# Optimization experiments

Hardware: AMD Instinct MI355X
Metric: run time of the kernel (lower is better)

The kernel has to match this reference:

```python
import jax, jax.numpy as jnp
import numpy as np
from jax import lax

B, C, H, W = 8, 64, 128, 128
KS = 3          # kernel size
K = KS * KS     # kernel field = 9
PAD = 1


def conv2d(x, w, b):
    # x: [B,Cin,H,W], w: [Cout,Cin,kh,kw], 'same' 3x3 conv
    y = lax.conv_general_dilated(x, w, window_strides=(1, 1),
                                 padding=((PAD, PAD), (PAD, PAD)),
                                 dimension_numbers=('NCHW', 'OIHW', 'NCHW'))
    return y + b[None, :, None, None]


def modulated_deform_conv(x, offset, mask, weight, bias):
    # x:[B,C,H,W], offset:[B,2K,H,W] (dy,dx per tap), mask:[B,K,H,W]
    Bs, Cin, Hin, Win = x.shape
    off = offset.reshape(Bs, K, 2, Hin, Win)
    ky, kx = jnp.meshgrid(jnp.arange(KS), jnp.arange(KS), indexing='ij')
    ky = ky.reshape(K).astype(x.dtype)   # kernel tap row offsets 0..2
    kx = kx.reshape(K).astype(x.dtype)
    # sampling positions p = p0 + p_k + offset (stride=1, pad=1)
    py = (jnp.arange(Hin, dtype=x.dtype)[None, None, :, None] - PAD
          + ky[None, :, None, None] + off[:, :, 0])            # [B,K,H,W]
    px = (jnp.arange(Win, dtype=x.dtype)[None, None, None, :] - PAD
          + kx[None, :, None, None] + off[:, :, 1])            # [B,K,H,W]

    y0 = jnp.floor(py); x0 = jnp.floor(px)
    ly = py - y0; lx = px - x0                                  # frac parts
    y0i = y0.astype(jnp.int32); x0i = x0.astype(jnp.int32)

    x_flat = x.reshape(Bs, Cin, Hin * Win)

    def gather(iy, ix):
        valid = ((iy >= 0) & (iy < Hin) & (ix >= 0) & (ix < Win))
        flat = (jnp.clip(iy, 0, Hin - 1) * Win + jnp.clip(ix, 0, Win - 1))
        g = jax.vmap(lambda xb, ib: xb[:, ib])(x_flat, flat.reshape(Bs, -1))
        g = g.reshape(Bs, Cin, K, Hin, Win)
        return g * valid[:, None].astype(x.dtype)

    w00 = ((1 - ly) * (1 - lx))[:, None]  # [B,1,K,H,W]
    w01 = ((1 - ly) * lx)[:, None]
    w10 = (ly * (1 - lx))[:, None]
    w11 = (ly * lx)[:, None]

    val = (w00 * gather(y0i, x0i) + w01 * gather(y0i, x0i + 1)
           + w10 * gather(y0i + 1, x0i) + w11 * gather(y0i + 1, x0i + 1))
    val = val * mask[:, None]                                   # modulation
    out = jnp.einsum('ock,bckhw->bohw', weight.reshape(weight.shape[0], Cin, K), val)
    return out + bias[None, :, None, None]


def setup_inputs() -> dict:
    key = jax.random.key(0)
    ks = jax.random.split(key, 7)
    s = 0.05
    return {
        'x': jax.random.normal(ks[0], (B, C, H, W), jnp.float32),
        'w_om': jax.random.normal(ks[1], (3 * K, C, KS, KS), jnp.float32) * s,
        'b_om': jax.random.normal(ks[2], (3 * K,), jnp.float32) * s,
        'w_dc': jax.random.normal(ks[3], (C, C, KS, KS), jnp.float32) * s,
        'b_dc': jax.random.normal(ks[4], (C,), jnp.float32) * s,
        'w_c': jax.random.normal(ks[5], (C, C, KS, KS), jnp.float32) * s,
        'b_c': jax.random.normal(ks[6], (C,), jnp.float32) * s,
    }


def reference(x, w_om, b_om, w_dc, b_dc, w_c, b_c):
    om = conv2d(x, w_om, b_om)                       # [B,3K,H,W]
    offset, mask_raw = om[:, :2 * K], om[:, 2 * K:]
    mask = 2.0 * jax.nn.sigmoid(mask_raw)
    out = modulated_deform_conv(x, offset, mask, w_dc, b_dc)
    act = jnp.where(out > 0, out, 0.2 * out)         # LeakyReLU(0.2)
    return conv2d(act, w_c, b_c) + x
```

## Files before the change

kernel.cpp:

```cpp
#include <hip/hip_runtime.h>
#include <math.h>

#define Bn 8
#define Cn 64
#define Hn 128
#define Wn 128
#define HWn (Hn * Wn)
#define Kn 9

#define XSW 36
#define XSROW (66 * XSW)
#define XSCC (3 * XSROW)
#define VSTRIDE 292

#define WOM_OFF 0
#define WDC_OFF 18432
#define WC_OFF 55296

typedef __attribute__((ext_vector_type(8))) short short8;
typedef __attribute__((ext_vector_type(4))) float floatx4;

__device__ __forceinline__ float bf2f(short s) {
  return __uint_as_float(((unsigned)(unsigned short)s) << 16);
}
__device__ __forceinline__ short f2bf(float f) {
  unsigned u = __float_as_uint(f);
  u += 0x7fff + ((u >> 16) & 1);
  return (short)(u >> 16);
}

__global__ __launch_bounds__(256) void k_prep_w(
    const float* __restrict__ w_om, const float* __restrict__ w_dc,
    const float* __restrict__ w_c, short* __restrict__ wt) {
  int idx = blockIdx.x * 256 + threadIdx.x;
  if (idx >= 92160) return;
  float v;
  if (idx < WDC_OFF) {
    int e = idx;
    int elem = e & 7, lane = (e >> 3) & 63, mt = (e >> 9) & 1, t = e >> 10;
    int kk = t % 9, cc = t / 9;
    int row = mt * 16 + (lane & 15);
    int cin = cc * 32 + (lane >> 4) * 8 + elem;
    v = (row < 27) ? w_om[(row * 64 + cin) * 9 + kk] : 0.f;
  } else {
    int e = (idx < WC_OFF) ? idx - WDC_OFF : idx - WC_OFF;
    const float* src = (idx < WC_OFF) ? w_dc : w_c;
    int elem = e & 7, lane = (e >> 3) & 63, mt = (e >> 9) & 3, t = e >> 11;
    int kk = t % 9, cc = t / 9;
    int row = mt * 16 + (lane & 15);
    int cin = cc * 32 + (lane >> 4) * 8 + elem;
    v = src[(row * 64 + cin) * 9 + kk];
  }
  wt[idx] = f2bf(v);
}

__global__ __launch_bounds__(256) void k_prep_x(const float* __restrict__ x,
                                                short* __restrict__ xT) {
  __shared__ float tile[64][129];
  const int bid = blockIdx.x;
  const int b = bid & 7, h = bid >> 3;
  const int tid = threadIdx.x;
  const float* xb = x + (size_t)b * 64 * HWn + h * Wn;
  for (int i = tid; i < 8192; i += 256) {
    int c = i >> 7, w = i & 127;
    tile[c][w] = xb[c * HWn + w];
  }
  __syncthreads();
  short* dst = xT + ((size_t)(b * Hn + h) * Wn) * 64;
  for (int i = tid; i < 2048; i += 256) {
    int w = i >> 4, c4 = (i & 15) * 4;
    short4 o;
    o.x = f2bf(tile[c4 + 0][w]);
    o.y = f2bf(tile[c4 + 1][w]);
    o.z = f2bf(tile[c4 + 2][w]);
    o.w = f2bf(tile[c4 + 3][w]);
    *(short4*)(dst + (size_t)w * 64 + c4) = o;
  }
}

__global__ __launch_bounds__(256, 3) void k_omdef(
    const short* __restrict__ xT, const short* __restrict__ wt,
    const float* __restrict__ b_om, const float* __restrict__ b_dc,
    short* __restrict__ actT) {
  __shared__ __attribute__((aligned(16))) char raw[64 * VSTRIDE * 2 + 9216];
  short* xs = (short*)raw;
  float* som = (float*)(raw + XSCC * 2);
  short(*val)[VSTRIDE] = (short(*)[VSTRIDE])raw;
  unsigned* sbw = (unsigned*)(raw + 64 * VSTRIDE * 2);
  unsigned* sb01 = sbw, *sb23 = sbw + 576, *sw01 = sbw + 1152,
          *sw23 = sbw + 1728;

  const int bid = blockIdx.x;
  const int b = bid & 7;
  const int r = bid >> 3;
  const int h = r >> 1, w0 = (r & 1) * 64;
  const int tid = threadIdx.x;
  const int wave = tid >> 6, lane = tid & 63, quad = lane >> 4, lr = lane & 15;
  const short* xb = xT + (size_t)b * HWn * 64;

  floatx4 zf = {0.f, 0.f, 0.f, 0.f};
  floatx4 aco0 = zf, aco1 = zf;
  const int mto = wave & 1;
  const int n0 = (wave >> 1) * 32;

  for (int cc = 0; cc < 2; ++cc) {
    if (cc) __syncthreads();
    for (int j = tid; j < 792; j += 256) {
      int c8 = (j & 3) * 8;
      int rr = j >> 2;
      int ky = rr / 66, p = rr - ky * 66;
      int gy = h + ky - 1, gx = w0 - 1 + p;
      short8 v = {0, 0, 0, 0, 0, 0, 0, 0};
      if (gy >= 0 && gy < Hn && gx >= 0 && gx < Wn)
        v = *(const short8*)(xb + (size_t)(gy * Wn + gx) * 64 + cc * 32 + c8);
      *(short8*)(xs + ky * XSROW + p * XSW + c8) = v;
    }
    __syncthreads();
#pragma unroll
    for (int kk = 0; kk < 9; ++kk) {
      int ky = kk / 3, kx = kk - ky * 3;
      short8 a = *(const short8*)(wt + WOM_OFF +
                                  (((cc * 9 + kk) * 2 + mto) * 64 + lane) * 8);
      const short* bp = xs + ky * XSROW + kx * XSW + quad * 8;
      short8 b0 = *(const short8*)(bp + (n0 + lr) * XSW);
      short8 b1 = *(const short8*)(bp + (n0 + 16 + lr) * XSW);
      aco0 = __builtin_amdgcn_mfma_f32_16x16x32_bf16(a, b0, aco0, 0, 0, 0);
      aco1 = __builtin_amdgcn_mfma_f32_16x16x32_bf16(a, b1, aco1, 0, 0, 0);
    }
  }
#pragma unroll
  for (int nt = 0; nt < 2; ++nt) {
    floatx4 a = nt ? aco1 : aco0;
    int px = n0 + nt * 16 + lr;
#pragma unroll
    for (int rr = 0; rr < 4; ++rr) {
      int co = mto * 16 + quad * 4 + rr;
      if (co < 27) {
        float v = a[rr] + b_om[co];
        if (co >= 18) v = 2.f / (1.f + expf(-v));
        som[co * 65 + px] = v;
      }
    }
  }
  __syncthreads();

  for (int pr = tid; pr < 576; pr += 256) {
    int k = pr >> 6, p = pr & 63;
    float offy = som[(2 * k) * 65 + p];
    float offx = som[(2 * k + 1) * 65 + p];
    float m = som[(18 + k) * 65 + p];
    float py = (float)(h - 1 + (k / 3)) + offy;
    float px_ = (float)(w0 + p - 1 + (k % 3)) + offx;
    float fy = floorf(py), fx = floorf(px_);
    float ly = py - fy, lx = px_ - fx;
    int iy0 = (int)fy, ix0 = (int)fx;
    int iy1 = iy0 + 1, ix1 = ix0 + 1;
    bool vy0 = (iy0 >= 0) && (iy0 < Hn);
    bool vy1 = (iy1 >= 0) && (iy1 < Hn);
    bool vx0 = (ix0 >= 0) && (ix0 < Wn);
    bool vx1 = (ix1 >= 0) && (ix1 < Wn);
    unsigned cy0 = (unsigned)min(max(iy0, 0), Hn - 1);
    unsigned cy1 = (unsigned)min(max(iy1, 0), Hn - 1);
    unsigned cx0 = (unsigned)min(max(ix0, 0), Wn - 1);
    unsigned cx1 = (unsigned)min(max(ix1, 0), Wn - 1);
    sb01[pr] = (cy0 * Wn + cx0) | ((cy0 * Wn + cx1) << 16);
    sb23[pr] = (cy1 * Wn + cx0) | ((cy1 * Wn + cx1) << 16);
    float u0 = (vy0 && vx0) ? (1.f - ly) * (1.f - lx) * m : 0.f;
    float u1 = (vy0 && vx1) ? (1.f - ly) * lx * m : 0.f;
    float u2 = (vy1 && vx0) ? ly * (1.f - lx) * m : 0.f;
    float u3 = (vy1 && vx1) ? ly * lx * m : 0.f;
    sw01[pr] = (unsigned)(unsigned short)f2bf(u0) |
               ((unsigned)(unsigned short)f2bf(u1) << 16);
    sw23[pr] = (unsigned)(unsigned short)f2bf(u2) |
               ((unsigned)(unsigned short)f2bf(u3) << 16);
  }
  __syncthreads();

  floatx4 acc[2][2] = {{zf, zf}, {zf, zf}};
  const int mt0 = (wave & 1) * 2;

  for (int cc = 0; cc < 2; ++cc) {
    if (cc) __syncthreads();
    for (int j = tid; j < 2304; j += 256) {
      int chunk = j & 3, pr = j >> 2;
      int p = pr & 63, k = pr >> 6;
      unsigned a01 = sb01[pr], a23 = sb23[pr];
      unsigned uw01 = sw01[pr], uw23 = sw23[pr];
      float u0 = bf2f((short)(uw01 & 0xFFFF));
      float u1 = bf2f((short)(uw01 >> 16));
      float u2 = bf2f((short)(uw23 & 0xFFFF));
      float u3 = bf2f((short)(uw23 >> 16));
      int co = cc * 32 + chunk * 8;
      short8 q0 = *(const short8*)(xb + (size_t)(a01 & 0xFFFF) * 64 + co);
      short8 q1 = *(const short8*)(xb + (size_t)(a01 >> 16) * 64 + co);
      short8 q2 = *(const short8*)(xb + (size_t)(a23 & 0xFFFF) * 64 + co);
      short8 q3 = *(const short8*)(xb + (size_t)(a23 >> 16) * 64 + co);
      short8 o;
#pragma unroll
      for (int e = 0; e < 8; ++e) {
        float f = u0 * bf2f(q0[e]) + u1 * bf2f(q1[e]) + u2 * bf2f(q2[e]) +
                  u3 * bf2f(q3[e]);
        o[e] = f2bf(f);
      }
      *(short8*)&val[p][k * 32 + chunk * 8] = o;
    }
    __syncthreads();
#pragma unroll
    for (int kk = 0; kk < 9; ++kk) {
      short8 a0 = *(const short8*)(wt + WDC_OFF +
                                   (((cc * 9 + kk) * 4 + mt0) * 64 + lane) * 8);
      short8 a1 = *(const short8*)(wt + WDC_OFF +
                                   (((cc * 9 + kk) * 4 + mt0 + 1) * 64 + lane) * 8);
      short8 b0 = *(const short8*)&val[n0 + lr][kk * 32 + quad * 8];
      short8 b1 = *(const short8*)&val[n0 + 16 + lr][kk * 32 + quad * 8];
      acc[0][0] = __builtin_amdgcn_mfma_f32_16x16x32_bf16(a0, b0, acc[0][0], 0, 0, 0);
      acc[0][1] = __builtin_amdgcn_mfma_f32_16x16x32_bf16(a0, b1, acc[0][1], 0, 0, 0);
      acc[1][0] = __builtin_amdgcn_mfma_f32_16x16x32_bf16(a1, b0, acc[1][0], 0, 0, 0);
      acc[1][1] = __builtin_amdgcn_mfma_f32_16x16x32_bf16(a1, b1, acc[1][1], 0, 0, 0);
    }
  }

  short* ab = actT + ((size_t)(b * Hn + h) * Wn + w0) * 64;
#pragma unroll
  for (int mt = 0; mt < 2; ++mt) {
#pragma unroll
    for (int nt = 0; nt < 2; ++nt) {
      int px = n0 + nt * 16 + lr;
      int c0 = (mt0 + mt) * 16 + quad * 4;
      short4 o;
      float v;
      v = acc[mt][nt][0] + b_dc[c0 + 0]; o.x = f2bf(v > 0.f ? v : 0.2f * v);
      v = acc[mt][nt][1] + b_dc[c0 + 1]; o.y = f2bf(v > 0.f ? v : 0.2f * v);
      v = acc[mt][nt][2] + b_dc[c0 + 2]; o.z = f2bf(v > 0.f ? v : 0.2f * v);
      v = acc[mt][nt][3] + b_dc[c0 + 3]; o.w = f2bf(v > 0.f ? v : 0.2f * v);
      *(short4*)(ab + (size_t)px * 64 + c0) = o;
    }
  }
}

__global__ __launch_bounds__(256, 5) void k_conv_out(
    const short* __restrict__ actT, const short* __restrict__ wt,
    const float* __restrict__ b_c, const float* __restrict__ x,
    float* __restrict__ out) {
  __shared__ __attribute__((aligned(16))) short as_[2 * XSCC];

  const int bid = blockIdx.x;
  const int b = bid & 7;
  const int r = bid >> 3;
  const int h = r >> 1, w0 = (r & 1) * 64;
  const int tid = threadIdx.x;
  const int wave = tid >> 6, lane = tid & 63, quad = lane >> 4, lr = lane & 15;
  const short* ab = actT + (size_t)b * HWn * 64;

  for (int j = tid; j < 1584; j += 256) {
    int cc = j / 792, rr = j - cc * 792;
    int c8 = (rr & 3) * 8;
    int r2 = rr >> 2;
    int ky = r2 / 66, p = r2 - ky * 66;
    int gy = h + ky - 1, gx = w0 - 1 + p;
    short8 v = {0, 0, 0, 0, 0, 0, 0, 0};
    if (gy >= 0 && gy < Hn && gx >= 0 && gx < Wn)
      v = *(const short8*)(ab + (size_t)(gy * Wn + gx) * 64 + cc * 32 + c8);
    *(short8*)(as_ + cc * XSCC + ky * XSROW + p * XSW + c8) = v;
  }
  __syncthreads();

  floatx4 zf = {0.f, 0.f, 0.f, 0.f};
  floatx4 acc[2][2] = {{zf, zf}, {zf, zf}};
  const int mt0 = (wave & 1) * 2;
  const int n0 = (wave >> 1) * 32;

  for (int cc = 0; cc < 2; ++cc) {
#pragma unroll
    for (int kk = 0; kk < 9; ++kk) {
      int ky = kk / 3, kx = kk - ky * 3;
      short8 a0 = *(const short8*)(wt + WC_OFF +
                                   (((cc * 9 + kk) * 4 + mt0) * 64 + lane) * 8);
      short8 a1 = *(const short8*)(wt + WC_OFF +
                                   (((cc * 9 + kk) * 4 + mt0 + 1) * 64 + lane) * 8);
      const short* bp = as_ + cc * XSCC + ky * XSROW + kx * XSW + quad * 8;
      short8 b0 = *(const short8*)(bp + (n0 + lr) * XSW);
      short8 b1 = *(const short8*)(bp + (n0 + 16 + lr) * XSW);
      acc[0][0] = __builtin_amdgcn_mfma_f32_16x16x32_bf16(a0, b0, acc[0][0], 0, 0, 0);
      acc[0][1] = __builtin_amdgcn_mfma_f32_16x16x32_bf16(a0, b1, acc[0][1], 0, 0, 0);
      acc[1][0] = __builtin_amdgcn_mfma_f32_16x16x32_bf16(a1, b0, acc[1][0], 0, 0, 0);
      acc[1][1] = __builtin_amdgcn_mfma_f32_16x16x32_bf16(a1, b1, acc[1][1], 0, 0, 0);
    }
  }

#pragma unroll
  for (int mt = 0; mt < 2; ++mt) {
#pragma unroll
    for (int nt = 0; nt < 2; ++nt) {
      int px = n0 + nt * 16 + lr;
#pragma unroll
      for (int rr = 0; rr < 4; ++rr) {
        int cout = (mt0 + mt) * 16 + quad * 4 + rr;
        size_t gidx = ((size_t)(b * 64 + cout) * Hn + h) * Wn + w0 + px;
        out[gidx] = acc[mt][nt][rr] + b_c[cout] + x[gidx];
      }
    }
  }
}

extern "C" void kernel_launch(void* const* d_in, const int* in_sizes, int n_in,
                              void* d_out, int out_size, void* d_ws,
                              size_t ws_size, hipStream_t stream) {
  const float* x = (const float*)d_in[0];
  const float* w_om = (const float*)d_in[1];
  const float* b_om = (const float*)d_in[2];
  const float* w_dc = (const float*)d_in[3];
  const float* b_dc = (const float*)d_in[4];
  const float* w_c = (const float*)d_in[5];
  const float* b_c = (const float*)d_in[6];
  float* out = (float*)d_out;

  short* xT = (short*)d_ws;
  short* actT = xT + (size_t)Bn * HWn * 64;
  short* wt = actT + (size_t)Bn * HWn * 64;

  k_prep_w<<<dim3(360), 256, 0, stream>>>(w_om, w_dc, w_c, wt);
  k_prep_x<<<dim3(1024), 256, 0, stream>>>(x, xT);
  k_omdef<<<dim3(2048), 256, 0, stream>>>(xT, wt, b_om, b_dc, actT);
  k_conv_out<<<dim3(2048), 256, 0, stream>>>(actT, wt, b_c, x, out);
}
```

Measured before the change: 237.5 us.

## Drop LDS staging; feed MFMA B operands directly from global memory per wave

Both the offset/mask conv, the deformable sampling GEMM and the output conv now load their B operands straight from global (channel-last bf16) into registers instead of staging halo tiles and the sampled value matrix in shared memory. Each wave owns 16 pixels and all output-channel tiles, so the bilinear-interpolated samples go directly into MFMA inputs without an LDS round trip and the intra-loop barriers disappear. Shared memory shrinks to the offset/mask and sample-index tables, and occupancy hints are raised to 4 blocks. The tradeoff is that overlapping 3x3 neighborhoods are re-read through cache instead of being reused from LDS, and weight fragments are loaded redundantly by every wave.

```diff
diff --git a/kernel.cpp b/kernel.cpp
--- a/kernel.cpp
+++ b/kernel.cpp
@@ -6,12 +6,6 @@
 #define Hn 128
 #define Wn 128
 #define HWn (Hn * Wn)
-#define Kn 9
-
-#define XSW 36
-#define XSROW (66 * XSW)
-#define XSCC (3 * XSROW)
-#define VSTRIDE 292
 
 #define WOM_OFF 0
 #define WDC_OFF 18432
@@ -78,17 +72,16 @@
   }
 }
 
-__global__ __launch_bounds__(256, 3) void k_omdef(
+__global__ __launch_bounds__(256, 4) void k_omdef(
     const short* __restrict__ xT, const short* __restrict__ wt,
     const float* __restrict__ b_om, const float* __restrict__ b_dc,
     short* __restrict__ actT) {
-  __shared__ __attribute__((aligned(16))) char raw[64 * VSTRIDE * 2 + 9216];
-  short* xs = (short*)raw;
-  float* som = (float*)(raw + XSCC * 2);
-  short(*val)[VSTRIDE] = (short(*)[VSTRIDE])raw;
-  unsigned* sbw = (unsigned*)(raw + 64 * VSTRIDE * 2);
-  unsigned* sb01 = sbw, *sb23 = sbw + 576, *sw01 = sbw + 1152,
-          *sw23 = sbw + 1728;
+  __shared__ float som[27 * 66];
+  __shared__ unsigned sbw[4 * 576];
+  unsigned* sb01 = sbw;
+  unsigned* sb23 = sbw + 576;
+  unsigned* sw01 = sbw + 1152;
+  unsigned* sw23 = sbw + 1728;
 
   const int bid = blockIdx.x;
   const int b = bid & 7;
@@ -97,48 +90,38 @@
   const int tid = threadIdx.x;
   const int wave = tid >> 6, lane = tid & 63, quad = lane >> 4, lr = lane & 15;
   const short* xb = xT + (size_t)b * HWn * 64;
+  const int pxl = wave * 16 + lr;
+  const int gxp = w0 + pxl;
 
   floatx4 zf = {0.f, 0.f, 0.f, 0.f};
-  floatx4 aco0 = zf, aco1 = zf;
-  const int mto = wave & 1;
-  const int n0 = (wave >> 1) * 32;
-
-  for (int cc = 0; cc < 2; ++cc) {
-    if (cc) __syncthreads();
-    for (int j = tid; j < 792; j += 256) {
-      int c8 = (j & 3) * 8;
-      int rr = j >> 2;
-      int ky = rr / 66, p = rr - ky * 66;
-      int gy = h + ky - 1, gx = w0 - 1 + p;
-      short8 v = {0, 0, 0, 0, 0, 0, 0, 0};
-      if (gy >= 0 && gy < Hn && gx >= 0 && gx < Wn)
-        v = *(const short8*)(xb + (size_t)(gy * Wn + gx) * 64 + cc * 32 + c8);
-      *(short8*)(xs + ky * XSROW + p * XSW + c8) = v;
-    }
-    __syncthreads();
-#pragma unroll
-    for (int kk = 0; kk < 9; ++kk) {
-      int ky = kk / 3, kx = kk - ky * 3;
-      short8 a = *(const short8*)(wt + WOM_OFF +
-                                  (((cc * 9 + kk) * 2 + mto) * 64 + lane) * 8);
-      const short* bp = xs + ky * XSROW + kx * XSW + quad * 8;
-      short8 b0 = *(const short8*)(bp + (n0 + lr) * XSW);
-      short8 b1 = *(const short8*)(bp + (n0 + 16 + lr) * XSW);
-      aco0 = __builtin_amdgcn_mfma_f32_16x16x32_bf16(a, b0, aco0, 0, 0, 0);
-      aco1 = __builtin_amdgcn_mfma_f32_16x16x32_bf16(a, b1, aco1, 0, 0, 0);
-    }
-  }
-#pragma unroll
-  for (int nt = 0; nt < 2; ++nt) {
-    floatx4 a = nt ? aco1 : aco0;
-    int px = n0 + nt * 16 + lr;
+
+  floatx4 aco[2] = {zf, zf};
+  for (int kk = 0; kk < 9; ++kk) {
+    int ky = kk / 3, kx = kk - ky * 3;
+    int gy = h + ky - 1, gx = gxp + kx - 1;
+    bool ok = ((unsigned)gy < (unsigned)Hn) && ((unsigned)gx < (unsigned)Wn);
+    int gyc = min(max(gy, 0), Hn - 1), gxc = min(max(gx, 0), Wn - 1);
+    const short* rec = xb + (size_t)(gyc * Wn + gxc) * 64 + quad * 8;
+#pragma unroll
+    for (int cc = 0; cc < 2; ++cc) {
+      short8 bf = *(const short8*)(rec + cc * 32);
+      if (!ok) bf = (short8){0, 0, 0, 0, 0, 0, 0, 0};
+      const short* ap = wt + WOM_OFF + (size_t)((cc * 9 + kk) * 2) * 512 + lane * 8;
+      short8 a0 = *(const short8*)(ap);
+      short8 a1 = *(const short8*)(ap + 512);
+      aco[0] = __builtin_amdgcn_mfma_f32_16x16x32_bf16(a0, bf, aco[0], 0, 0, 0);
+      aco[1] = __builtin_amdgcn_mfma_f32_16x16x32_bf16(a1, bf, aco[1], 0, 0, 0);
+    }
+  }
+#pragma unroll
+  for (int mt = 0; mt < 2; ++mt) {
 #pragma unroll
     for (int rr = 0; rr < 4; ++rr) {
-      int co = mto * 16 + quad * 4 + rr;
+      int co = mt * 16 + quad * 4 + rr;
       if (co < 27) {
-        float v = a[rr] + b_om[co];
+        float v = aco[mt][rr] + b_om[co];
         if (co >= 18) v = 2.f / (1.f + expf(-v));
-        som[co * 65 + px] = v;
+        som[co * 66 + pxl] = v;
       }
     }
   }
@@ -146,9 +129,9 @@
 
   for (int pr = tid; pr < 576; pr += 256) {
     int k = pr >> 6, p = pr & 63;
-    float offy = som[(2 * k) * 65 + p];
-    float offx = som[(2 * k + 1) * 65 + p];
-    float m = som[(18 + k) * 65 + p];
+    float offy = som[(2 * k) * 66 + p];
+    float offx = som[(2 * k + 1) * 66 + p];
+    float m = som[(18 + k) * 66 + p];
     float py = (float)(h - 1 + (k / 3)) + offy;
     float px_ = (float)(w0 + p - 1 + (k % 3)) + offx;
     float fy = floorf(py), fx = floorf(px_);
@@ -176,74 +159,59 @@
   }
   __syncthreads();
 
-  floatx4 acc[2][2] = {{zf, zf}, {zf, zf}};
-  const int mt0 = (wave & 1) * 2;
-
-  for (int cc = 0; cc < 2; ++cc) {
-    if (cc) __syncthreads();
-    for (int j = tid; j < 2304; j += 256) {
-      int chunk = j & 3, pr = j >> 2;
-      int p = pr & 63, k = pr >> 6;
-      unsigned a01 = sb01[pr], a23 = sb23[pr];
-      unsigned uw01 = sw01[pr], uw23 = sw23[pr];
-      float u0 = bf2f((short)(uw01 & 0xFFFF));
-      float u1 = bf2f((short)(uw01 >> 16));
-      float u2 = bf2f((short)(uw23 & 0xFFFF));
-      float u3 = bf2f((short)(uw23 >> 16));
-      int co = cc * 32 + chunk * 8;
-      short8 q0 = *(const short8*)(xb + (size_t)(a01 & 0xFFFF) * 64 + co);
-      short8 q1 = *(const short8*)(xb + (size_t)(a01 >> 16) * 64 + co);
-      short8 q2 = *(const short8*)(xb + (size_t)(a23 & 0xFFFF) * 64 + co);
-      short8 q3 = *(const short8*)(xb + (size_t)(a23 >> 16) * 64 + co);
-      short8 o;
+  floatx4 acc[4] = {zf, zf, zf, zf};
+  for (int kk = 0; kk < 9; ++kk) {
+    int pr = kk * 64 + pxl;
+    unsigned a01 = sb01[pr], a23 = sb23[pr];
+    unsigned uw01 = sw01[pr], uw23 = sw23[pr];
+    float u0 = bf2f((short)(uw01 & 0xFFFF));
+    float u1 = bf2f((short)(uw01 >> 16));
+    float u2 = bf2f((short)(uw23 & 0xFFFF));
+    float u3 = bf2f((short)(uw23 >> 16));
+    const short* s0 = xb + (size_t)(a01 & 0xFFFF) * 64 + quad * 8;
+    const short* s1 = xb + (size_t)(a01 >> 16) * 64 + quad * 8;
+    const short* s2 = xb + (size_t)(a23 & 0xFFFF) * 64 + quad * 8;
+    const short* s3 = xb + (size_t)(a23 >> 16) * 64 + quad * 8;
+#pragma unroll
+    for (int cc = 0; cc < 2; ++cc) {
+      short8 q0 = *(const short8*)(s0 + cc * 32);
+      short8 q1 = *(const short8*)(s1 + cc * 32);
+      short8 q2 = *(const short8*)(s2 + cc * 32);
+      short8 q3 = *(const short8*)(s3 + cc * 32);
+      short8 bf;
 #pragma unroll
       for (int e = 0; e < 8; ++e) {
         float f = u0 * bf2f(q0[e]) + u1 * bf2f(q1[e]) + u2 * bf2f(q2[e]) +
                   u3 * bf2f(q3[e]);
-        o[e] = f2bf(f);
-      }
-      *(short8*)&val[p][k * 32 + chunk * 8] = o;
-    }
-    __syncthreads();
-#pragma unroll
-    for (int kk = 0; kk < 9; ++kk) {
-      short8 a0 = *(const short8*)(wt + WDC_OFF +
-                                   (((cc * 9 + kk) * 4 + mt0) * 64 + lane) * 8);
-      short8 a1 = *(const short8*)(wt + WDC_OFF +
-                                   (((cc * 9 + kk) * 4 + mt0 + 1) * 64 + lane) * 8);
-      short8 b0 = *(const short8*)&val[n0 + lr][kk * 32 + quad * 8];
-      short8 b1 = *(const short8*)&val[n0 + 16 + lr][kk * 32 + quad * 8];
-      acc[0][0] = __builtin_amdgcn_mfma_f32_16x16x32_bf16(a0, b0, acc[0][0], 0, 0, 0);
-      acc[0][1] = __builtin_amdgcn_mfma_f32_16x16x32_bf16(a0, b1, acc[0][1], 0, 0, 0);
-      acc[1][0] = __builtin_amdgcn_mfma_f32_16x16x32_bf16(a1, b0, acc[1][0], 0, 0, 0);
-      acc[1][1] = __builtin_amdgcn_mfma_f32_16x16x32_bf16(a1, b1, acc[1][1], 0, 0, 0);
+        bf[e] = f2bf(f);
+      }
+      const short* ap = wt + WDC_OFF + (size_t)((cc * 9 + kk) * 4) * 512 + lane * 8;
+#pragma unroll
+      for (int mt = 0; mt < 4; ++mt) {
+        short8 am = *(const short8*)(ap + mt * 512);
+        acc[mt] = __builtin_amdgcn_mfma_f32_16x16x32_bf16(am, bf, acc[mt], 0, 0, 0);
+      }
     }
   }
 
   short* ab = actT + ((size_t)(b * Hn + h) * Wn + w0) * 64;
 #pragma unroll
-  for (int mt = 0; mt < 2; ++mt) {
-#pragma unroll
-    for (int nt = 0; nt < 2; ++nt) {
-      int px = n0 + nt * 16 + lr;
-      int c0 = (mt0 + mt) * 16 + quad * 4;
-      short4 o;
-      float v;
-      v = acc[mt][nt][0] + b_dc[c0 + 0]; o.x = f2bf(v > 0.f ? v : 0.2f * v);
-      v = acc[mt][nt][1] + b_dc[c0 + 1]; o.y = f2bf(v > 0.f ? v : 0.2f * v);
-      v = acc[mt][nt][2] + b_dc[c0 + 2]; o.z = f2bf(v > 0.f ? v : 0.2f * v);
-      v = acc[mt][nt][3] + b_dc[c0 + 3]; o.w = f2bf(v > 0.f ? v : 0.2f * v);
-      *(short4*)(ab + (size_t)px * 64 + c0) = o;
-    }
-  }
-}
-
-__global__ __launch_bounds__(256, 5) void k_conv_out(
+  for (int mt = 0; mt < 4; ++mt) {
+    int c0 = mt * 16 + quad * 4;
+    short4 o;
+    float v;
+    v = acc[mt][0] + b_dc[c0 + 0]; o.x = f2bf(v > 0.f ? v : 0.2f * v);
+    v = acc[mt][1] + b_dc[c0 + 1]; o.y = f2bf(v > 0.f ? v : 0.2f * v);
+    v = acc[mt][2] + b_dc[c0 + 2]; o.z = f2bf(v > 0.f ? v : 0.2f * v);
+    v = acc[mt][3] + b_dc[c0 + 3]; o.w = f2bf(v > 0.f ? v : 0.2f * v);
+    *(short4*)(ab + (size_t)pxl * 64 + c0) = o;
+  }
+}
+
+__global__ __launch_bounds__(256, 4) void k_conv_out(
     const short* __restrict__ actT, const short* __restrict__ wt,
     const float* __restrict__ b_c, const float* __restrict__ x,
     float* __restrict__ out) {
-  __shared__ __attribute__((aligned(16))) short as_[2 * XSCC];
-
   const int bid = blockIdx.x;
   const int b = bid & 7;
   const int r = bid >> 3;
@@ -251,54 +219,37 @@
   const int tid = threadIdx.x;
   const int wave = tid >> 6, lane = tid & 63, quad = lane >> 4, lr = lane & 15;
   const short* ab = actT + (size_t)b * HWn * 64;
-
-  for (int j = tid; j < 1584; j += 256) {
-    int cc = j / 792, rr = j - cc * 792;
-    int c8 = (rr & 3) * 8;
-    int r2 = rr >> 2;
-    int ky = r2 / 66, p = r2 - ky * 66;
-    int gy = h + ky - 1, gx = w0 - 1 + p;
-    short8 v = {0, 0, 0, 0, 0, 0, 0, 0};
-    if (gy >= 0 && gy < Hn && gx >= 0 && gx < Wn)
-      v = *(const short8*)(ab + (size_t)(gy * Wn + gx) * 64 + cc * 32 + c8);
-    *(short8*)(as_ + cc * XSCC + ky * XSROW + p * XSW + c8) = v;
-  }
-  __syncthreads();
+  const int pxl = wave * 16 + lr;
+  const int gxp = w0 + pxl;
 
   floatx4 zf = {0.f, 0.f, 0.f, 0.f};
-  floatx4 acc[2][2] = {{zf, zf}, {zf, zf}};
-  const int mt0 = (wave & 1) * 2;
-  const int n0 = (wave >> 1) * 32;
-
-  for (int cc = 0; cc < 2; ++cc) {
-#pragma unroll
-    for (int kk = 0; kk < 9; ++kk) {
-      int ky = kk / 3, kx = kk - ky * 3;
-      short8 a0 = *(const short8*)(wt + WC_OFF +
-                                   (((cc * 9 + kk) * 4 + mt0) * 64 + lane) * 8);
-      short8 a1 = *(const short8*)(wt + WC_OFF +
-                                   (((cc * 9 + kk) * 4 + mt0 + 1) * 64 + lane) * 8);
-      const short* bp = as_ + cc * XSCC + ky * XSROW + kx * XSW + quad * 8;
-      short8 b0 = *(const short8*)(bp + (n0 + lr) * XSW);
-      short8 b1 = *(const short8*)(bp + (n0 + 16 + lr) * XSW);
-      acc[0][0] = __builtin_amdgcn_mfma_f32_16x16x32_bf16(a0, b0, acc[0][0], 0, 0, 0);
-      acc[0][1] = __builtin_amdgcn_mfma_f32_16x16x32_bf16(a0, b1, acc[0][1], 0, 0, 0);
-      acc[1][0] = __builtin_amdgcn_mfma_f32_16x16x32_bf16(a1, b0, acc[1][0], 0, 0, 0);
-      acc[1][1] = __builtin_amdgcn_mfma_f32_16x16x32_bf16(a1, b1, acc[1][1], 0, 0, 0);
-    }
-  }
-
-#pragma unroll
-  for (int mt = 0; mt < 2; ++mt) {
-#pragma unroll
-    for (int nt = 0; nt < 2; ++nt) {
-      int px = n0 + nt * 16 + lr;
-#pragma unroll
-      for (int rr = 0; rr < 4; ++rr) {
-        int cout = (mt0 + mt) * 16 + quad * 4 + rr;
-        size_t gidx = ((size_t)(b * 64 + cout) * Hn + h) * Wn + w0 + px;
-        out[gidx] = acc[mt][nt][rr] + b_c[cout] + x[gidx];
-      }
+  floatx4 acc[4] = {zf, zf, zf, zf};
+  for (int kk = 0; kk < 9; ++kk) {
+    int ky = kk / 3, kx = kk - ky * 3;
+    int gy = h + ky - 1, gx = gxp + kx - 1;
+    bool ok = ((unsigned)gy < (unsigned)Hn) && ((unsigned)gx < (unsigned)Wn);
+    int gyc = min(max(gy, 0), Hn - 1), gxc = min(max(gx, 0), Wn - 1);
+    const short* rec = ab + (size_t)(gyc * Wn + gxc) * 64 + quad * 8;
+#pragma unroll
+    for (int cc = 0; cc < 2; ++cc) {
+      short8 bf = *(const short8*)(rec + cc * 32);
+      if (!ok) bf = (short8){0, 0, 0, 0, 0, 0, 0, 0};
+      const short* ap = wt + WC_OFF + (size_t)((cc * 9 + kk) * 4) * 512 + lane * 8;
+#pragma unroll
+      for (int mt = 0; mt < 4; ++mt) {
+        short8 am = *(const short8*)(ap + mt * 512);
+        acc[mt] = __builtin_amdgcn_mfma_f32_16x16x32_bf16(am, bf, acc[mt], 0, 0, 0);
+      }
+    }
+  }
+
+#pragma unroll
+  for (int mt = 0; mt < 4; ++mt) {
+#pragma unroll
+    for (int rr = 0; rr < 4; ++rr) {
+      int cout = mt * 16 + quad * 4 + rr;
+      size_t gidx = ((size_t)(b * 64 + cout) * Hn + h) * Wn + w0 + pxl;
+      out[gidx] = acc[mt][rr] + b_c[cout] + x[gidx];
     }
   }
 }
```

New measurement: 244.3 us. +2.9%, slower.
